# Kernel optimization log

Measured on AMD Instinct MI355X. Metric: run time of the kernel, lower is better.

The kernel has to match this reference:

```python
import jax, jax.numpy as jnp
import numpy as np

EMBED_DIM = 512
PATCH = 16
QUANT_N = 1024
QUANT_DIM = 256
LN_EPS = 1e-5


def setup_inputs() -> dict:
    key = jax.random.key(0)
    k1, k2, k3, k4 = jax.random.split(key, 4)
    B, T, M = 16, 8192, 128
    fbank = jax.random.normal(k1, (B, T, M), dtype=jnp.float32)
    # xavier-normal conv weight (O,I,kH,kW), frozen in the original module
    fan = PATCH * PATCH + EMBED_DIM
    conv_w = jax.random.normal(k2, (EMBED_DIM, 1, PATCH, PATCH), dtype=jnp.float32) * np.sqrt(2.0 / fan)
    proj = jax.random.normal(k3, (EMBED_DIM, QUANT_DIM), dtype=jnp.float32) * np.sqrt(2.0 / (EMBED_DIM + QUANT_DIM))
    codebook = jax.random.normal(k4, (QUANT_N, QUANT_DIM), dtype=jnp.float32)
    return {"fbank": fbank, "conv_w": conv_w, "proj": proj, "codebook": codebook}


def _l2norm(x, eps=1e-12):
    return x / jnp.maximum(jnp.linalg.norm(x, axis=-1, keepdims=True), eps)


def reference(fbank, conv_w, proj, codebook):
    # patch embedding: Conv2d(1, D, k=16, s=16) over (B, 1, T, mel)
    x = fbank[:, None, :, :]  # B,1,T,M
    feats = jax.lax.conv_general_dilated(
        x, conv_w, window_strides=(PATCH, PATCH), padding='VALID',
        dimension_numbers=('NCHW', 'OIHW', 'NCHW'))  # B,D,T/16,M/16
    B, D, H, W = feats.shape
    feats = feats.reshape(B, D, H * W).transpose(0, 2, 1)  # B,N,D
    # LayerNorm without affine
    mu = jnp.mean(feats, axis=-1, keepdims=True)
    var = jnp.var(feats, axis=-1, keepdims=True)
    feats = (feats - mu) * jax.lax.rsqrt(var + LN_EPS)
    # random projection quantizer: l2norm(x @ P) vs l2-normalized codebook;
    # argmin euclidean distance == argmax cosine similarity for unit vectors
    p = _l2norm(jnp.einsum('bnd,dq->bnq', feats, proj))  # B,N,Q
    cb = _l2norm(codebook)                                # K,Q
    sim = jnp.einsum('bnq,kq->bnk', p, cb)                # B,N,K
    embed_ind = jnp.argmax(sim, axis=-1)                  # B,N int
    return embed_ind
```

## Files before the change

kernel.cpp:

```cpp
#include <hip/hip_runtime.h>
#include <math.h>

#define QD 256
#define QN 1024
#define TT 8192

typedef __bf16 bf16x8 __attribute__((ext_vector_type(8)));
typedef float  f32x16 __attribute__((ext_vector_type(16)));
typedef unsigned short ushort_t;
typedef unsigned short us8 __attribute__((ext_vector_type(8)));

#define PL  0
#define MU_ 49152
#define LM_ 51200
#define T2_ 51328
#define TR_ 51456
#define CN_ 51584
#define CC_ 51712
#define SMEM_TOTAL 55808

__device__ __forceinline__ void split3(float x, ushort_t& h, ushort_t& m, ushort_t& l) {
    unsigned int xu = __float_as_uint(x);
    h = (ushort_t)(xu >> 16);
    float hf = __uint_as_float(xu & 0xFFFF0000u);
    float r1 = x - hf;
    unsigned int r1u = __float_as_uint(r1);
    m = (ushort_t)(r1u >> 16);
    float mf = __uint_as_float(r1u & 0xFFFF0000u);
    float r2 = r1 - mf;
    l = (ushort_t)(__float_as_uint(r2) >> 16);
}
__device__ __forceinline__ f32x16 MF(bf16x8 a, bf16x8 b, f32x16 c) {
    return __builtin_amdgcn_mfma_f32_32x32x16_bf16(a, b, c, 0, 0, 0);
}
__device__ __forceinline__ unsigned fenc(float f) {
    unsigned u = __float_as_uint(f);
    return (u & 0x80000000u) ? ~u : (u | 0x80000000u);
}
__device__ __forceinline__ float fdec(unsigned u) {
    return (u & 0x80000000u) ? __uint_as_float(u ^ 0x80000000u) : __uint_as_float(~u);
}

__global__ __launch_bounds__(256) void k_pre(const float* __restrict__ convw,
                                             const float* __restrict__ proj,
                                             const float* __restrict__ cb,
                                             ushort_t* __restrict__ cbph,
                                             float* __restrict__ cbn,
                                             ushort_t* __restrict__ w2p,
                                             float* __restrict__ wsum,
                                             float* __restrict__ p1) {
    int bx = blockIdx.x, t = threadIdx.x;
    if (bx < 256) {
        int c = bx*4 + (t>>6), lane = t&63;
        float4 v = ((const float4*)(cb + (size_t)c*QD))[lane];
        float ss = v.x*v.x + v.y*v.y + v.z*v.z + v.w*v.w;
        #pragma unroll
        for (int off = 32; off > 0; off >>= 1) ss += __shfl_down(ss, off);
        ss = __shfl(ss, 0);
        float inv = 1.0f/fmaxf(sqrtf(ss), 1e-12f);
        float4 vn = make_float4(v.x*inv, v.y*inv, v.z*inv, v.w*inv);
        *(float4*)(cbn + (size_t)c*QD + 4*lane) = vn;
        float vals[4] = {vn.x, vn.y, vn.z, vn.w};
        #pragma unroll
        for (int i = 0; i < 4; ++i) {
            int k = 4*lane + i;
            size_t base = ((size_t)(k>>4)*32 + (c>>5))*512 + (((k>>3)&1)*32 + (c&31))*8 + (k&7);
            cbph[base] = (ushort_t)(__float_as_uint(vals[i]) >> 16);
        }
    } else if (bx < 320) {
        int col0 = (bx - 256) * 4;
        __shared__ float4 colv4[512];
        const float* src = proj + col0;
        colv4[t]       = *(const float4*)(src + (size_t)t * 256);
        colv4[t + 256] = *(const float4*)(src + (size_t)(t + 256) * 256);
        __syncthreads();
        float a0 = 0.f, a1 = 0.f, a2 = 0.f, a3 = 0.f;
        #pragma unroll 16
        for (int d = 0; d < 512; ++d) {
            float wv = convw[d*256 + t];
            float4 cv = colv4[d];
            a0 += wv*cv.x; a1 += wv*cv.y; a2 += wv*cv.z; a3 += wv*cv.w;
        }
        float accs[4] = {a0, a1, a2, a3};
        #pragma unroll
        for (int j = 0; j < 4; ++j) {
            int col = col0 + j;
            ushort_t hb, mb, lb; split3(accs[j], hb, mb, lb);
            size_t base = ((size_t)(t>>4)*8 + (col>>5))*512 + (((t>>3)&1)*32 + (col&31))*8 + (t&7);
            w2p[base] = hb;
            w2p[base + 65536] = mb;
            w2p[base + 131072] = lb;
        }
    } else if (bx == 320) {
        float s = 0.f;
        #pragma unroll 32
        for (int d = 0; d < 512; ++d) s += convw[d*256 + t];
        wsum[t] = s;
    } else {
        float s = 0.f;
        #pragma unroll 32
        for (int d = 0; d < 512; ++d) s += proj[d*256 + t];
        p1[t] = s;
    }
}

__global__ __launch_bounds__(512)
__attribute__((amdgpu_waves_per_eu(4, 4)))
void k_mega(const float* __restrict__ fbank,
            const ushort_t* __restrict__ w2p,
            const ushort_t* __restrict__ cbph,
            const float* __restrict__ cbn,
            const float* __restrict__ wsum,
            const float* __restrict__ p1,
            int* __restrict__ out) {
    __shared__ char smem[SMEM_TOTAL];
    float*    muS   = (float*)(smem + MU_);
    float*    lnMuS = (float*)(smem + LM_);
    float*    tn2A  = (float*)(smem + T2_);
    unsigned* thrR  = (unsigned*)(smem + TR_);
    int*      cntS  = (int*)(smem + CN_);
    ushort_t* candS = (ushort_t*)(smem + CC_);

    int tid = threadIdx.x;
    int n0 = blockIdx.x * 32;
    int w = tid >> 6, lane = tid & 63;
    int n31 = lane & 31, h = lane >> 5;
    size_t loff = (size_t)lane * 16;
    const char* w2pc = (const char*)w2p;
    const char* cbhc = (const char*)cbph;

    auto loadB1 = [&](int kcv, bf16x8 (&dst)[3]) {
        #pragma unroll
        for (int q = 0; q < 3; ++q)
            dst[q] = *(const bf16x8*)(w2pc + (size_t)q*131072 + (size_t)(kcv*8 + w)*1024 + loff);
    };
    auto loadB2 = [&](int kcv, bf16x8 (&dst)[4]) {
        dst[0] = *(const bf16x8*)(cbhc + (size_t)(kcv*32 + w     )*1024 + loff);
        dst[1] = *(const bf16x8*)(cbhc + (size_t)(kcv*32 + w + 8 )*1024 + loff);
        dst[2] = *(const bf16x8*)(cbhc + (size_t)(kcv*32 + w + 16)*1024 + loff);
        dst[3] = *(const bf16x8*)(cbhc + (size_t)(kcv*32 + w + 24)*1024 + loff);
    };
    auto loadA = [&](int kcv, bf16x8 (&a)[3]) {
        #pragma unroll
        for (int p = 0; p < 3; ++p)
            a[p] = *(const bf16x8*)(smem + p*16384 + kcv*1024 + loff);
    };
    auto compute6 = [&](bf16x8 (&a)[3], bf16x8 (&b)[3], f32x16& acc) {
        acc = MF(a[0], b[0], acc);
        acc = MF(a[0], b[1], acc);
        acc = MF(a[1], b[0], acc);
        acc = MF(a[1], b[1], acc);
        acc = MF(a[0], b[2], acc);
        acc = MF(a[2], b[0], acc);
    };

    float4 va[2], vb[2];
    #pragma unroll
    for (int i = 0; i < 2; ++i) {
        int id = tid + 512*i;
        int kc = id >> 6, cl = id & 63;
        int tok = cl & 31, hh2 = cl >> 5;
        int n = n0 + tok;
        int b = n >> 12, r = n & 4095, th = r >> 3, wm = r & 7;
        const float* src = fbank + ((size_t)(b*TT + th*16 + kc))*128 + wm*16 + hh2*8;
        va[i] = ((const float4*)src)[0];
        vb[i] = ((const float4*)src)[1];
    }
    int kc0 = tid >> 6, hh0 = (tid >> 5) & 1;
    int wb0 = 16*kc0 + 8*hh0;
    float4 w00 = *(const float4*)(wsum + wb0);
    float4 w01 = *(const float4*)(wsum + wb0 + 4);
    float4 w10 = *(const float4*)(wsum + wb0 + 128);
    float4 w11 = *(const float4*)(wsum + wb0 + 132);
    float p1v = p1[32*w + n31];

    bf16x8 B1b[3][3];
    loadB1(0, B1b[0]);
    loadB1(1, B1b[1]);

    if (tid < 32) { tn2A[tid] = 0.f; thrR[tid] = 0u; cntS[tid] = 0; }

    float wsv[2][8];
    wsv[0][0]=w00.x; wsv[0][1]=w00.y; wsv[0][2]=w00.z; wsv[0][3]=w00.w;
    wsv[0][4]=w01.x; wsv[0][5]=w01.y; wsv[0][6]=w01.z; wsv[0][7]=w01.w;
    wsv[1][0]=w10.x; wsv[1][1]=w10.y; wsv[1][2]=w10.z; wsv[1][3]=w10.w;
    wsv[1][4]=w11.x; wsv[1][5]=w11.y; wsv[1][6]=w11.z; wsv[1][7]=w11.w;

    float mupart = 0.f;
    #pragma unroll
    for (int i = 0; i < 2; ++i) {
        int id = tid + 512*i;
        int kc = id >> 6, cl = id & 63;
        float vals[8] = {va[i].x, va[i].y, va[i].z, va[i].w, vb[i].x, vb[i].y, vb[i].z, vb[i].w};
        us8 hv, mv, lv;
        #pragma unroll
        for (int j = 0; j < 8; ++j) {
            ushort_t a_, b_, c_; split3(vals[j], a_, b_, c_);
            hv[j] = a_; mv[j] = b_; lv[j] = c_;
            mupart += vals[j] * wsv[i][j];
        }
        char* cp = smem + kc*1024 + cl*16;
        *(us8*)cp = hv;
        *(us8*)(cp + 16384) = mv;
        *(us8*)(cp + 32768) = lv;
    }
    muS[(tid>>5)*32 + (tid&31)] = mupart;
    __syncthreads();

    if (tid < 32) {
        float pm = 0.f;
        #pragma unroll
        for (int s = 0; s < 16; ++s) pm += muS[s*32 + tid];
        lnMuS[tid] = pm * (1.f/512.f);
    }

    f32x16 accE, accO;
    #pragma unroll
    for (int r2 = 0; r2 < 16; ++r2) { accE[r2] = 0.f; accO[r2] = 0.f; }
    #pragma unroll
    for (int kc = 0; kc < 16; ++kc) {
        if (kc < 14) loadB1(kc + 2, B1b[(kc + 2) % 3]);
        bf16x8 a[3]; loadA(kc, a);
        if (kc & 1) compute6(a, B1b[kc % 3], accO);
        else        compute6(a, B1b[kc % 3], accE);
    }

    bf16x8 qA[4], qB[4];
    loadB2(0, qA);

    __syncthreads();

    {
        int q = 32*w + n31;
        #pragma unroll
        for (int reg = 0; reg < 16; ++reg) {
            int tok = (reg&3) + 8*(reg>>2) + 4*h;
            float tv = (accE[reg] + accO[reg]) - lnMuS[tok]*p1v;
            *(float*)(smem + 16384 + tok*1024 + q*4) = tv;
            *(ushort_t*)(smem + (q>>4)*1024 + (((q>>3)&1)*32 + tok)*16 + (q&7)*2)
                = (ushort_t)(__float_as_uint(tv) >> 16);
            float sq2 = tv*tv;
            #pragma unroll
            for (int msk = 1; msk < 32; msk <<= 1) sq2 += __shfl_xor(sq2, msk);
            if (n31 == 0) atomicAdd(&tn2A[tok], sq2);
        }
    }
    __syncthreads();

    f32x16 s0, s1, s2, s3;
    #pragma unroll
    for (int r2 = 0; r2 < 16; ++r2) { s0[r2]=0.f; s1[r2]=0.f; s2[r2]=0.f; s3[r2]=0.f; }
    for (int kc = 0; kc < 16; kc += 2) {
        loadB2(kc + 1, qB);
        {
            bf16x8 ah = *(const bf16x8*)(smem + kc*1024 + loff);
            s0 = MF(ah, qA[0], s0); s1 = MF(ah, qA[1], s1);
            s2 = MF(ah, qA[2], s2); s3 = MF(ah, qA[3], s3);
        }
        if (kc + 2 < 16) loadB2(kc + 2, qA);
        {
            bf16x8 ah = *(const bf16x8*)(smem + (kc+1)*1024 + loff);
            s0 = MF(ah, qB[0], s0); s1 = MF(ah, qB[1], s1);
            s2 = MF(ah, qB[2], s2); s3 = MF(ah, qB[3], s3);
        }
    }
    #pragma unroll
    for (int reg = 0; reg < 16; ++reg) {
        int tok = (reg&3) + 8*(reg>>2) + 4*h;
        float m = fmaxf(fmaxf(s0[reg], s1[reg]), fmaxf(s2[reg], s3[reg]));
        #pragma unroll
        for (int msk = 1; msk < 32; msk <<= 1) m = fmaxf(m, __shfl_xor(m, msk));
        if (n31 == 0) atomicMax(&thrR[tok], fenc(m));
    }
    __syncthreads();

    #pragma unroll
    for (int reg = 0; reg < 16; ++reg) {
        int tok = (reg&3) + 8*(reg>>2) + 4*h;
        float th_ = fdec(thrR[tok]) - 0.04f*sqrtf(tn2A[tok]);
        if (s0[reg] >= th_) { int p = atomicAdd(&cntS[tok], 1); if (p < 64) candS[tok*64 + p] = (ushort_t)(32*(w     ) + n31); }
        if (s1[reg] >= th_) { int p = atomicAdd(&cntS[tok], 1); if (p < 64) candS[tok*64 + p] = (ushort_t)(32*(w + 8 ) + n31); }
        if (s2[reg] >= th_) { int p = atomicAdd(&cntS[tok], 1); if (p < 64) candS[tok*64 + p] = (ushort_t)(32*(w + 16) + n31); }
        if (s3[reg] >= th_) { int p = atomicAdd(&cntS[tok], 1); if (p < 64) candS[tok*64 + p] = (ushort_t)(32*(w + 24) + n31); }
    }
    __syncthreads();

    #pragma unroll 1
    for (int tk = 0; tk < 4; ++tk) {
        int tok = 4*w + tk;
        float4 tv = *(const float4*)(smem + 16384 + tok*1024 + lane*16);
        int nc = cntS[tok];
        bool full = (nc > 64);
        if (full) nc = 1024;
        float bv = -3.4e38f; int bi = 0x7fffffff;
        int c0 = full ? 0 : (int)candS[tok*64];
        float4 v0 = *(const float4*)(cbn + (size_t)c0*256 + 4*lane);
        int c1 = c0; float4 v1 = v0;
        if (nc > 1) {
            c1 = full ? 1 : (int)candS[tok*64 + 1];
            v1 = *(const float4*)(cbn + (size_t)c1*256 + 4*lane);
        }
        for (int c = 0; c < nc; ++c) {
            int c2 = c0; float4 v2 = v0;
            if (c + 2 < nc) {
                c2 = full ? (c + 2) : (int)candS[tok*64 + c + 2];
                v2 = *(const float4*)(cbn + (size_t)c2*256 + 4*lane);
            }
            float d = v0.x*tv.x + v0.y*tv.y + v0.z*tv.z + v0.w*tv.w;
            #pragma unroll
            for (int msk = 1; msk < 64; msk <<= 1) d += __shfl_xor(d, msk);
            if (d > bv || (d == bv && c0 < bi)) { bv = d; bi = c0; }
            c0 = c1; v0 = v1; c1 = c2; v1 = v2;
        }
        if (lane == 0) out[n0 + tok] = bi;
    }
}

extern "C" void kernel_launch(void* const* d_in, const int* in_sizes, int n_in,
                              void* d_out, int out_size, void* d_ws, size_t ws_size,
                              hipStream_t stream) {
    const float* fbank = (const float*)d_in[0];
    const float* convw = (const float*)d_in[1];
    const float* proj  = (const float*)d_in[2];
    const float* cbook = (const float*)d_in[3];
    int* out = (int*)d_out;

    char* ws = (char*)d_ws;
    ushort_t* cbph = (ushort_t*)ws;
    float* cbn     = (float*)(ws + 0x080000);
    ushort_t* w2p  = (ushort_t*)(ws + 0x180000);
    float* wsum    = (float*)(ws + 0x1E0000);
    float* p1      = (float*)(ws + 0x1E1000);

    hipLaunchKernelGGL(k_pre,  dim3(322),  dim3(256), 0, stream,
                       convw, proj, cbook, cbph, cbn, w2p, wsum, p1);
    hipLaunchKernelGGL(k_mega, dim3(2048), dim3(512), 0, stream,
                       fbank, w2p, cbph, cbn, wsum, p1, out);
}
```

Baseline: 328.4 us.

## Stage wsum/p1 in LDS, replace shared atomics with per-wave partials, double-buffer B loads

After: 337.0 us. 1.03x slower.

```diff
diff --git a/kernel.cpp b/kernel.cpp
--- a/kernel.cpp
+++ b/kernel.cpp
@@ -11,13 +11,16 @@
 typedef unsigned short us8 __attribute__((ext_vector_type(8)));
 
 #define PL  0
-#define MU_ 49152
-#define LM_ 51200
-#define T2_ 51328
-#define TR_ 51456
-#define CN_ 51584
-#define CC_ 51712
-#define SMEM_TOTAL 55808
+#define WS_ 49152
+#define P1_ 50176
+#define MU_ 51200
+#define LM_ 53248
+#define TN_ 53376
+#define LX_ 54400
+#define TH_ 55424
+#define CN_ 55552
+#define CC_ 55680
+#define SMEM_TOTAL 59776
 
 __device__ __forceinline__ void split3(float x, ushort_t& h, ushort_t& m, ushort_t& l) {
     unsigned int xu = __float_as_uint(x);
@@ -32,13 +35,6 @@
 }
 __device__ __forceinline__ f32x16 MF(bf16x8 a, bf16x8 b, f32x16 c) {
     return __builtin_amdgcn_mfma_f32_32x32x16_bf16(a, b, c, 0, 0, 0);
-}
-__device__ __forceinline__ unsigned fenc(float f) {
-    unsigned u = __float_as_uint(f);
-    return (u & 0x80000000u) ? ~u : (u | 0x80000000u);
-}
-__device__ __forceinline__ float fdec(unsigned u) {
-    return (u & 0x80000000u) ? __uint_as_float(u ^ 0x80000000u) : __uint_as_float(~u);
 }
 
 __global__ __launch_bounds__(256) void k_pre(const float* __restrict__ convw,
@@ -104,21 +100,22 @@
     }
 }
 
-__global__ __launch_bounds__(512)
-__attribute__((amdgpu_waves_per_eu(4, 4)))
-void k_mega(const float* __restrict__ fbank,
-            const ushort_t* __restrict__ w2p,
-            const ushort_t* __restrict__ cbph,
-            const float* __restrict__ cbn,
-            const float* __restrict__ wsum,
-            const float* __restrict__ p1,
-            int* __restrict__ out) {
+__global__ __launch_bounds__(512, 4) void k_mega(const float* __restrict__ fbank,
+                                                 const ushort_t* __restrict__ w2p,
+                                                 const ushort_t* __restrict__ cbph,
+                                                 const float* __restrict__ cbn,
+                                                 const float* __restrict__ wsum,
+                                                 const float* __restrict__ p1,
+                                                 int* __restrict__ out) {
     __shared__ char smem[SMEM_TOTAL];
-    float*    muS   = (float*)(smem + MU_);
-    float*    lnMuS = (float*)(smem + LM_);
-    float*    tn2A  = (float*)(smem + T2_);
-    unsigned* thrR  = (unsigned*)(smem + TR_);
-    int*      cntS  = (int*)(smem + CN_);
+    float* wsS   = (float*)(smem + WS_);
+    float* p1S   = (float*)(smem + P1_);
+    float* muS   = (float*)(smem + MU_);
+    float* lnMuS = (float*)(smem + LM_);
+    float* tn2P  = (float*)(smem + TN_);
+    float* lmaxS = (float*)(smem + LX_);
+    float* thrS  = (float*)(smem + TH_);
+    int*   cntS  = (int*)(smem + CN_);
     ushort_t* candS = (ushort_t*)(smem + CC_);
 
     int tid = threadIdx.x;
@@ -166,44 +163,33 @@
         va[i] = ((const float4*)src)[0];
         vb[i] = ((const float4*)src)[1];
     }
-    int kc0 = tid >> 6, hh0 = (tid >> 5) & 1;
-    int wb0 = 16*kc0 + 8*hh0;
-    float4 w00 = *(const float4*)(wsum + wb0);
-    float4 w01 = *(const float4*)(wsum + wb0 + 4);
-    float4 w10 = *(const float4*)(wsum + wb0 + 128);
-    float4 w11 = *(const float4*)(wsum + wb0 + 132);
-    float p1v = p1[32*w + n31];
-
-    bf16x8 B1b[3][3];
-    loadB1(0, B1b[0]);
-    loadB1(1, B1b[1]);
-
-    if (tid < 32) { tn2A[tid] = 0.f; thrR[tid] = 0u; cntS[tid] = 0; }
-
-    float wsv[2][8];
-    wsv[0][0]=w00.x; wsv[0][1]=w00.y; wsv[0][2]=w00.z; wsv[0][3]=w00.w;
-    wsv[0][4]=w01.x; wsv[0][5]=w01.y; wsv[0][6]=w01.z; wsv[0][7]=w01.w;
-    wsv[1][0]=w10.x; wsv[1][1]=w10.y; wsv[1][2]=w10.z; wsv[1][3]=w10.w;
-    wsv[1][4]=w11.x; wsv[1][5]=w11.y; wsv[1][6]=w11.z; wsv[1][7]=w11.w;
+    if (tid < 256) wsS[tid] = wsum[tid];
+    else           p1S[tid - 256] = p1[tid - 256];
+    __syncthreads();
 
     float mupart = 0.f;
     #pragma unroll
     for (int i = 0; i < 2; ++i) {
         int id = tid + 512*i;
         int kc = id >> 6, cl = id & 63;
+        int hh2 = cl >> 5;
         float vals[8] = {va[i].x, va[i].y, va[i].z, va[i].w, vb[i].x, vb[i].y, vb[i].z, vb[i].w};
         us8 hv, mv, lv;
         #pragma unroll
         for (int j = 0; j < 8; ++j) {
             ushort_t a_, b_, c_; split3(vals[j], a_, b_, c_);
             hv[j] = a_; mv[j] = b_; lv[j] = c_;
-            mupart += vals[j] * wsv[i][j];
+            mupart += vals[j] * wsS[16*kc + 8*hh2 + j];
         }
         char* cp = smem + kc*1024 + cl*16;
         *(us8*)cp = hv;
         *(us8*)(cp + 16384) = mv;
         *(us8*)(cp + 32768) = lv;
     }
+
+    bf16x8 bA[3], bB[3];
+    loadB1(0, bA);
+
     muS[(tid>>5)*32 + (tid&31)] = mupart;
     __syncthreads();
 
@@ -217,12 +203,11 @@
     f32x16 accE, accO;
     #pragma unroll
     for (int r2 = 0; r2 < 16; ++r2) { accE[r2] = 0.f; accO[r2] = 0.f; }
-    #pragma unroll
-    for (int kc = 0; kc < 16; ++kc) {
-        if (kc < 14) loadB1(kc + 2, B1b[(kc + 2) % 3]);
-        bf16x8 a[3]; loadA(kc, a);
-        if (kc & 1) compute6(a, B1b[kc % 3], accO);
-        else        compute6(a, B1b[kc % 3], accE);
+    for (int kc = 0; kc < 16; kc += 2) {
+        loadB1(kc + 1, bB);
+        { bf16x8 a[3]; loadA(kc, a); compute6(a, bA, accE); }
+        if (kc + 2 < 16) loadB1(kc + 2, bA);
+        { bf16x8 a[3]; loadA(kc + 1, a); compute6(a, bB, accO); }
     }
 
     bf16x8 qA[4], qB[4];
@@ -232,6 +217,7 @@
 
     {
         int q = 32*w + n31;
+        float p1v = p1S[q];
         #pragma unroll
         for (int reg = 0; reg < 16; ++reg) {
             int tok = (reg&3) + 8*(reg>>2) + 4*h;
@@ -242,7 +228,7 @@
             float sq2 = tv*tv;
             #pragma unroll
             for (int msk = 1; msk < 32; msk <<= 1) sq2 += __shfl_xor(sq2, msk);
-            if (n31 == 0) atomicAdd(&tn2A[tok], sq2);
+            if (n31 == 0) tn2P[tok*8 + w] = sq2;
         }
     }
     __syncthreads();
@@ -270,21 +256,27 @@
         float m = fmaxf(fmaxf(s0[reg], s1[reg]), fmaxf(s2[reg], s3[reg]));
         #pragma unroll
         for (int msk = 1; msk < 32; msk <<= 1) m = fmaxf(m, __shfl_xor(m, msk));
-        if (n31 == 0) atomicMax(&thrR[tok], fenc(m));
-    }
-    __syncthreads();
-
+        if (n31 == 0) lmaxS[tok*8 + w] = m;
+    }
+    __syncthreads();
+    if (tid < 32) {
+        float g = -3.4e38f, sq = 0.f;
+        #pragma unroll
+        for (int p = 0; p < 8; ++p) { g = fmaxf(g, lmaxS[tid*8 + p]); sq += tn2P[tid*8 + p]; }
+        thrS[tid] = g - 0.04f*sqrtf(sq);
+        cntS[tid] = 0;
+    }
+    __syncthreads();
     #pragma unroll
     for (int reg = 0; reg < 16; ++reg) {
         int tok = (reg&3) + 8*(reg>>2) + 4*h;
-        float th_ = fdec(thrR[tok]) - 0.04f*sqrtf(tn2A[tok]);
+        float th_ = thrS[tok];
         if (s0[reg] >= th_) { int p = atomicAdd(&cntS[tok], 1); if (p < 64) candS[tok*64 + p] = (ushort_t)(32*(w     ) + n31); }
         if (s1[reg] >= th_) { int p = atomicAdd(&cntS[tok], 1); if (p < 64) candS[tok*64 + p] = (ushort_t)(32*(w + 8 ) + n31); }
         if (s2[reg] >= th_) { int p = atomicAdd(&cntS[tok], 1); if (p < 64) candS[tok*64 + p] = (ushort_t)(32*(w + 16) + n31); }
         if (s3[reg] >= th_) { int p = atomicAdd(&cntS[tok], 1); if (p < 64) candS[tok*64 + p] = (ushort_t)(32*(w + 24) + n31); }
     }
     __syncthreads();
-
     #pragma unroll 1
     for (int tk = 0; tk < 4; ++tk) {
         int tok = 4*w + tk;
```
